# Performance work log

Hardware: AMD Instinct MI355X
Metric: run time of the kernel (lower is better)

Reference implementation:

```python
import jax, jax.numpy as jnp
import numpy as np

DIM = 768
NUM_HEADS = 12
HEAD_DIM = DIM // NUM_HEADS


def setup_inputs() -> dict:
    key = jax.random.key(0)
    k1, k2, k3 = jax.random.split(key, 3)
    B, N, C = 8, 4096, DIM
    x = jax.random.normal(k1, (B, N, C), dtype=jnp.float32)
    # torch nn.Linear weights are (out_features, in_features)
    W_qkv = jax.random.normal(k2, (3 * C, C), dtype=jnp.float32) * 0.02
    b_qkv = jnp.zeros((3 * C,), dtype=jnp.float32)
    W_proj = jax.random.normal(k3, (C, C), dtype=jnp.float32) * 0.02
    b_proj = jnp.zeros((C,), dtype=jnp.float32)
    return {"x": x, "W_qkv": W_qkv, "b_qkv": b_qkv, "W_proj": W_proj, "b_proj": b_proj}


def reference(x, W_qkv, b_qkv, W_proj, b_proj):
    B, N, C = x.shape
    H, D = NUM_HEADS, HEAD_DIM
    # qkv projection -> (3, B, H, N, D)
    qkv = (x @ W_qkv.T + b_qkv).reshape(B, N, 3, H, D).transpose(2, 0, 3, 1, 4)
    q, k, v = qkv[0], qkv[1], qkv[2]
    # feature map: elu(x) + 1 (positive kernel features)
    q = jax.nn.elu(q) + 1.0
    k = jax.nn.elu(k) + 1.0
    # kernelized linear attention: (K^T V) then Q (K^T V)
    kv = jnp.einsum('bhnd,bhnv->bhdv', k, v)          # (B,H,D,D)
    out = jnp.einsum('bhnd,bhdv->bhnv', q, kv)        # (B,H,N,D)
    k_sum = k.sum(axis=2)                             # (B,H,D)
    normalizer = jnp.einsum('bhnd,bhd->bhn', q, k_sum) + 1e-06
    out = out / normalizer[..., None]
    out = out.transpose(0, 2, 1, 3).reshape(B, N, C)
    out = out @ W_proj.T + b_proj
    return out
```

## Files before the change

### kernel.cpp

```cpp
#include <hip/hip_runtime.h>
#include <hip/hip_fp16.h>
#include <math.h>

#define NHEADS 12
#define SEQ 4096
#define BATCH 8

typedef _Float16 half8 __attribute__((ext_vector_type(8)));
typedef float floatx4 __attribute__((ext_vector_type(4)));

__global__ void zero_kernel(float* p, int n) {
  int i = blockIdx.x * 256 + threadIdx.x;
  if (i < n) p[i] = 0.f;
}

__global__ void cast_f2h(const float* __restrict__ in, __half* __restrict__ out, int n) {
  int i = (blockIdx.x * 256 + threadIdx.x) * 4;
  if (i < n) {
    float4 v = *(const float4*)&in[i];
    ushort4 o;
    o.x = __half_as_ushort(__float2half(v.x));
    o.y = __half_as_ushort(__float2half(v.y));
    o.z = __half_as_ushort(__float2half(v.z));
    o.w = __half_as_ushort(__float2half(v.w));
    *(ushort4*)&out[i] = o;
  }
}

__device__ __forceinline__ void stage_tile(const __half* __restrict__ gbase, int ldg,
                                           _Float16* lds, int t) {
#pragma unroll
  for (int it = 0; it < 2; ++it) {
    const int s  = it * 256 + t;
    const int mp = s >> 3, ps = s & 7;
    const int p  = ps ^ (mp & 7);
    const int r  = mp * 2 + (p >> 2);
    const int q  = p & 3;
    const __half* g = gbase + (size_t)r * ldg + q * 8;
    _Float16* dst = lds + (s >> 6) * 512;
    __builtin_amdgcn_global_load_lds((const __attribute__((address_space(1))) void*)g,
                                     (__attribute__((address_space(3))) void*)dst, 16, 0, 0);
  }
}
__device__ __forceinline__ void stage_blk(const __half* __restrict__ gbase, int ldg,
                                          _Float16* lds, int t) {
  const int mp = t >> 3, ps = t & 7;
  const int p  = ps ^ (mp & 7);
  const int r  = mp * 2 + (p >> 2);
  const int q  = p & 3;
  const __half* g = gbase + (size_t)r * ldg + q * 8;
  _Float16* dst = lds + (t >> 6) * 512;
  __builtin_amdgcn_global_load_lds((const __attribute__((address_space(1))) void*)g,
                                   (__attribute__((address_space(3))) void*)dst, 16, 0, 0);
}
__device__ __forceinline__ half8 read_frag(const _Float16* lds, int row, int quad) {
  const int mp = row >> 1;
  const int p  = ((row & 1) << 2) | quad;
  const int ps = p ^ (mp & 7);
  return *(const half8*)(lds + (mp * 8 + ps) * 8);
}

__device__ __forceinline__ void write_l64(_Float16* lds, int row, int col, float v) {
  lds[row * 64 + ((((col >> 3) ^ (row & 7))) << 3) + (col & 7)] = (_Float16)v;
}
__device__ __forceinline__ half8 read_l64c(const _Float16* lds, int row, int c) {
  return *(const half8*)(lds + row * 64 + ((c ^ (row & 7)) << 3));
}

__device__ __forceinline__ void barrier_raw() {
  asm volatile("s_barrier" ::: "memory");
}

template<int MODE>
__global__ __launch_bounds__(512, 2) void hgemm256_kernel(
    const __half* __restrict__ A, const __half* __restrict__ W,
    const float* __restrict__ bias,
    __half* __restrict__ outK, __half* __restrict__ outV,
    float* __restrict__ outF, int colBase)
{
  const int K = 768;
  const int NT = 24;
  extern __shared__ __align__(16) _Float16 sh[];
  const int t    = threadIdx.x;
  const int w    = t >> 6;
  const int l    = t & 63;
  const int quad = l >> 4;
  const int mrow = l & 15;
  const int wm   = w >> 2;
  const int wn   = w & 3;

  constexpr int JB = (MODE == 1) ? 6 : 3;
  const int bid  = blockIdx.x;
  const int xcd  = bid & 7;
  const int ii   = bid >> 3;
  const int mg   = ii / JB;
  const int jj   = ii - mg * JB;
  const int m0   = (xcd * 16 + mg) * 256;
  const int j0   = jj * 256;

  floatx4 acc[8][4];
#pragma unroll
  for (int i = 0; i < 8; ++i)
#pragma unroll
    for (int j = 0; j < 4; ++j) acc[i][j] = (floatx4){0.f, 0.f, 0.f, 0.f};

#pragma unroll
  for (int kt = 0; kt < 3; ++kt) {
    _Float16* db = sh + kt * 16384;
    const int kg = kt * 32;
    stage_blk(A + (size_t)m0 * K + kg, K, db, t);
    stage_blk(A + (size_t)(m0 + 128) * K + kg, K, db + 4096, t);
    stage_blk(W + (size_t)(colBase + j0) * K + kg, K, db + 8192, t);
    stage_blk(W + (size_t)(colBase + j0 + 128) * K + kg, K, db + 12288, t);
  }
  asm volatile("s_waitcnt vmcnt(8)" ::: "memory");
  barrier_raw();

#pragma unroll 4
  for (int kt = 0; kt < NT; ++kt) {
    const _Float16* bb = sh + (kt & 3) * 16384;
    const bool st = (kt + 3 < NT);
    _Float16* db = sh + ((kt + 3) & 3) * 16384;
    const int kg = (kt + 3) * 32;
    half8 af[4], bf[4];

#pragma unroll
    for (int j = 0; j < 4; ++j) {
      const int C = wn * 64 + j * 16 + mrow;
      bf[j] = read_frag(bb + 8192 + (C >> 7) * 4096, C & 127, quad);
    }
#pragma unroll
    for (int i = 0; i < 4; ++i)
      af[i] = read_frag(bb + wm * 4096, i * 16 + mrow, quad);
    if (st) {
      stage_blk(A + (size_t)m0 * K + kg, K, db, t);
      stage_blk(A + (size_t)(m0 + 128) * K + kg, K, db + 4096, t);
    }
#pragma unroll
    for (int i = 0; i < 4; ++i)
#pragma unroll
      for (int j = 0; j < 4; ++j)
        acc[i][j] = __builtin_amdgcn_mfma_f32_16x16x32_f16(af[i], bf[j], acc[i][j], 0, 0, 0);

#pragma unroll
    for (int i = 0; i < 4; ++i)
      af[i] = read_frag(bb + wm * 4096, (i + 4) * 16 + mrow, quad);
    if (st) {
      stage_blk(W + (size_t)(colBase + j0) * K + kg, K, db + 8192, t);
      stage_blk(W + (size_t)(colBase + j0 + 128) * K + kg, K, db + 12288, t);
    }
#pragma unroll
    for (int i = 0; i < 4; ++i)
#pragma unroll
      for (int j = 0; j < 4; ++j)
        acc[i + 4][j] = __builtin_amdgcn_mfma_f32_16x16x32_f16(af[i], bf[j], acc[i + 4][j], 0, 0, 0);

    if (kt < NT - 3)       asm volatile("s_waitcnt vmcnt(8)" ::: "memory");
    else if (kt == NT - 3) asm volatile("s_waitcnt vmcnt(4)" ::: "memory");
    else if (kt == NT - 2) asm volatile("s_waitcnt vmcnt(0)" ::: "memory");
    barrier_raw();
  }

  if (MODE == 0) {
#pragma unroll
    for (int j = 0; j < 4; ++j) {
      const int col = j0 + wn * 64 + j * 16 + mrow;
      const float bsv = bias[col];
#pragma unroll
      for (int i = 0; i < 8; ++i)
#pragma unroll
        for (int r = 0; r < 4; ++r) {
          const int m = m0 + wm * 128 + i * 16 + quad * 4 + r;
          outF[(size_t)m * 768 + col] = acc[i][j][r] + bsv;
        }
    }
    return;
  }

  const int col0 = colBase + j0 + wn * 64;
  const int t3   = col0 / 768;
  const int h    = (col0 - t3 * 768) >> 6;
  __half* dst    = (t3 == 1) ? outK : outV;
  const int m0w  = m0 + wm * 128;
  const int b_   = m0w >> 12;
  const int n0w  = m0w & 4095;
  _Float16* scr  = sh + w * 4096;

#pragma unroll
  for (int hf = 0; hf < 2; ++hf) {
#pragma unroll
    for (int j = 0; j < 4; ++j) {
      const int col = j * 16 + mrow;
      const float bsv = bias[col0 + col];
#pragma unroll
      for (int ii2 = 0; ii2 < 4; ++ii2)
#pragma unroll
        for (int r = 0; r < 4; ++r) {
          const int row = ii2 * 16 + quad * 4 + r;
          float val = acc[hf * 4 + ii2][j][r] + bsv;
          if (t3 == 1) val = (val > 0.f) ? (val + 1.f) : expf(val);
          write_l64(scr, row, col, val);
        }
    }
    barrier_raw();
    const size_t gb = ((size_t)(b_ * NHEADS + h) * SEQ + n0w + hf * 64) * 64;
#pragma unroll
    for (int it = 0; it < 8; ++it) {
      const int row = it * 8 + (l >> 3);
      const int c   = l & 7;
      half8 vv = read_l64c(scr, row, c);
      *(half8*)((_Float16*)dst + gb + (size_t)row * 64 + c * 8) = vv;
    }
    barrier_raw();
  }
}

__global__ __launch_bounds__(256) void kv_kernel(
    const __half* __restrict__ k, const __half* __restrict__ v,
    float* __restrict__ kv, float* __restrict__ ksum)
{
  __shared__ float ks[32 * 64];
  __shared__ float vs[32 * 64];
  const int bh = blockIdx.x;
  const int s  = blockIdx.y;
  const int t  = threadIdx.x;
  const int w  = t >> 6;
  const int l  = t & 63;
  const size_t base = (size_t)bh * SEQ * 64 + (size_t)s * 512 * 64;

  float acc[16];
#pragma unroll
  for (int i = 0; i < 16; ++i) acc[i] = 0.f;
  float kspart = 0.f;

  const int nn0 = t >> 3;
  const int c8  = (t & 7) * 8;

  for (int chunk = 0; chunk < 512; chunk += 32) {
    __syncthreads();
    {
      half8 kk = *(const half8*)&k[base + (size_t)(chunk + nn0) * 64 + c8];
      half8 vv = *(const half8*)&v[base + (size_t)(chunk + nn0) * 64 + c8];
#pragma unroll
      for (int e = 0; e < 8; ++e) {
        ks[nn0 * 64 + c8 + e] = (float)kk[e];
        vs[nn0 * 64 + c8 + e] = (float)vv[e];
      }
    }
    __syncthreads();
#pragma unroll 4
    for (int nn = 0; nn < 32; ++nn) {
      const float ve = vs[nn * 64 + l];
      const float4* kr = (const float4*)&ks[nn * 64 + w * 16];
      float4 k0 = kr[0], k1 = kr[1], k2 = kr[2], k3 = kr[3];
      acc[0]  += k0.x * ve; acc[1]  += k0.y * ve; acc[2]  += k0.z * ve; acc[3]  += k0.w * ve;
      acc[4]  += k1.x * ve; acc[5]  += k1.y * ve; acc[6]  += k1.z * ve; acc[7]  += k1.w * ve;
      acc[8]  += k2.x * ve; acc[9]  += k2.y * ve; acc[10] += k2.z * ve; acc[11] += k2.w * ve;
      acc[12] += k3.x * ve; acc[13] += k3.y * ve; acc[14] += k3.z * ve; acc[15] += k3.w * ve;
      kspart += ks[nn * 64 + l];
    }
  }
#pragma unroll
  for (int i = 0; i < 16; ++i) {
    const int d = w * 16 + i;
    atomicAdd(&kv[((size_t)bh * 64 + d) * 64 + l], acc[i]);
  }
  if (t < 64) atomicAdd(&ksum[(size_t)bh * 64 + l], kspart);
}

__global__ __launch_bounds__(256) void qattn_kernel(
    const __half* __restrict__ A, const __half* __restrict__ W,
    const float* __restrict__ bias,
    const float* __restrict__ kvg, const float* __restrict__ ksumg,
    __half* __restrict__ att)
{
  const int K = 768;
  __shared__ __align__(16) _Float16 sh[24576];
  _Float16* As = sh;
  _Float16* Bs = sh + 4096;
  __shared__ float norms[256];
  __shared__ float ksums[128];
  const int t    = threadIdx.x;
  const int w    = t >> 6;
  const int l    = t & 63;
  const int quad = l >> 4;
  const int mrow = l & 15;
  const int m0   = blockIdx.x * 128;
  const int j0   = blockIdx.y * 128;
  const int wr   = (w >> 1) * 64;
  const int wc   = (w & 1) * 64;
  const int b_   = m0 >> 12;
  const int h0   = j0 >> 6;

  {
    _Float16* kvT0 = sh + 16384;
#pragma unroll
    for (int ii = 0; ii < 32; ++ii) {
      const int gidx = ii * 256 + t;
      const int head = gidx >> 12;
      const int r    = gidx & 4095;
      const float val = kvg[(size_t)(b_ * NHEADS + h0 + head) * 4096 + r];
      write_l64(kvT0 + head * 4096, r & 63, r >> 6, val);
    }
    if (t < 128) ksums[t] = ksumg[(size_t)(b_ * NHEADS + h0 + (t >> 6)) * 64 + (t & 63)];
  }

  floatx4 acc[4][4];
#pragma unroll
  for (int i = 0; i < 4; ++i)
#pragma unroll
    for (int j = 0; j < 4; ++j) acc[i][j] = (floatx4){0.f, 0.f, 0.f, 0.f};

  for (int k0 = 0; k0 < K; k0 += 32) {
    __syncthreads();
    stage_tile(A + (size_t)m0 * K + k0, K, As, t);
    stage_tile(W + (size_t)j0 * K + k0, K, Bs, t);
    __syncthreads();
    half8 af[4], bf[4];
#pragma unroll
    for (int i = 0; i < 4; ++i) af[i] = read_frag(As, wr + i * 16 + mrow, quad);
#pragma unroll
    for (int j = 0; j < 4; ++j) bf[j] = read_frag(Bs, wc + j * 16 + mrow, quad);
#pragma unroll
    for (int i = 0; i < 4; ++i)
#pragma unroll
      for (int j = 0; j < 4; ++j)
        acc[i][j] = __builtin_amdgcn_mfma_f32_16x16x32_f16(af[i], bf[j], acc[i][j], 0, 0, 0);
  }

  _Float16* qtile = sh + w * 4096;
  const _Float16* kvT = sh + 16384 + (w & 1) * 4096;
  const int hh = w & 1;

  __syncthreads();
#pragma unroll
  for (int j = 0; j < 4; ++j) {
    const int col = j * 16 + mrow;
    const float bsv = bias[j0 + wc + col];
#pragma unroll
    for (int i = 0; i < 4; ++i)
#pragma unroll
      for (int r = 0; r < 4; ++r) {
        const int row = i * 16 + quad * 4 + r;
        float val = acc[i][j][r] + bsv;
        val = (val > 0.f) ? (val + 1.f) : expf(val);
        write_l64(qtile, row, col, val);
      }
  }
  __syncthreads();

  {
    float nrm = 0.f;
#pragma unroll
    for (int c = 0; c < 8; ++c) {
      half8 qv = read_l64c(qtile, l, c);
#pragma unroll
      for (int e = 0; e < 8; ++e) nrm += (float)qv[e] * ksums[hh * 64 + c * 8 + e];
    }
    norms[w * 64 + l] = 1.f / (nrm + 1e-6f);
  }

  floatx4 oacc[4][4];
#pragma unroll
  for (int i = 0; i < 4; ++i)
#pragma unroll
    for (int j = 0; j < 4; ++j) oacc[i][j] = (floatx4){0.f, 0.f, 0.f, 0.f};
#pragma unroll
  for (int ks = 0; ks < 2; ++ks) {
    half8 af[4], bf[4];
#pragma unroll
    for (int i = 0; i < 4; ++i) af[i] = read_l64c(qtile, i * 16 + mrow, ks * 4 + quad);
#pragma unroll
    for (int j = 0; j < 4; ++j) bf[j] = read_l64c(kvT, j * 16 + mrow, ks * 4 + quad);
#pragma unroll
    for (int i = 0; i < 4; ++i)
#pragma unroll
      for (int j = 0; j < 4; ++j)
        oacc[i][j] = __builtin_amdgcn_mfma_f32_16x16x32_f16(af[i], bf[j], oacc[i][j], 0, 0, 0);
  }
  __syncthreads();

#pragma unroll
  for (int i = 0; i < 4; ++i)
#pragma unroll
    for (int r = 0; r < 4; ++r) {
      const int row = i * 16 + quad * 4 + r;
      const float rn = norms[w * 64 + row];
#pragma unroll
      for (int j = 0; j < 4; ++j)
        write_l64(qtile, row, j * 16 + mrow, oacc[i][j][r] * rn);
    }
  __syncthreads();
  const int n0w = (m0 & 4095) + wr;
  const size_t abase = (size_t)(b_ * SEQ + n0w) * 768 + (h0 + hh) * 64;
#pragma unroll
  for (int it = 0; it < 8; ++it) {
    const int row = it * 8 + (l >> 3);
    const int c   = l & 7;
    half8 vv = read_l64c(qtile, row, c);
    *(half8*)((_Float16*)att + abase + (size_t)row * 768 + c * 8) = vv;
  }
}

extern "C" void kernel_launch(void* const* d_in, const int* in_sizes, int n_in,
                              void* d_out, int out_size, void* d_ws, size_t ws_size,
                              hipStream_t stream)
{
  const float* x     = (const float*)d_in[0];
  const float* Wqkv  = (const float*)d_in[1];
  const float* bqkv  = (const float*)d_in[2];
  const float* Wproj = (const float*)d_in[3];
  const float* bproj = (const float*)d_in[4];
  float* out = (float*)d_out;

  const size_t SZ = (size_t)BATCH * NHEADS * SEQ * 64;
  __half* xh  = (__half*)d_ws;
  __half* Wqh = xh + SZ;
  __half* Wph = Wqh + (size_t)2304 * 768;
  __half* R3  = Wph + (size_t)768 * 768;
  __half* R4  = R3 + SZ;
  float*  kvb = (float*)(R4 + SZ);
  float*  ksum = kvb + 96 * 64 * 64;

  static bool attr_set = false;
  if (!attr_set) {
    hipFuncSetAttribute((const void*)hgemm256_kernel<1>,
                        hipFuncAttributeMaxDynamicSharedMemorySize, 131072);
    hipFuncSetAttribute((const void*)hgemm256_kernel<0>,
                        hipFuncAttributeMaxDynamicSharedMemorySize, 131072);
    attr_set = true;
  }

  zero_kernel<<<1560, 256, 0, stream>>>(kvb, 96 * 64 * 64 + 96 * 64);

  cast_f2h<<<(int)(SZ / 1024), 256, 0, stream>>>(x, xh, (int)SZ);
  cast_f2h<<<(2304 * 768) / 1024, 256, 0, stream>>>(Wqkv, Wqh, 2304 * 768);
  cast_f2h<<<(768 * 768) / 1024, 256, 0, stream>>>(Wproj, Wph, 768 * 768);

  hgemm256_kernel<1><<<768, 512, 131072, stream>>>(
      xh, Wqh, bqkv, R3, R4, nullptr, 768);

  kv_kernel<<<dim3(96, 8), 256, 0, stream>>>(R3, R4, kvb, ksum);

  qattn_kernel<<<dim3(256, 6), 256, 0, stream>>>(
      xh, Wqh, bqkv, kvb, ksum, R3);

  hgemm256_kernel<0><<<384, 512, 131072, stream>>>(
      R3, Wph, bproj, nullptr, nullptr, out, 0);
}
```

Measured before the change: 479.5 us.

## Store K/V transposed and compute K^T V with MFMA instructions

The QKV GEMM epilogue now writes K and V in a transposed (head-dim major, sequence minor) layout. A new kv kernel reads that layout directly into MFMA fp16 fragments and computes K^T V, plus the K row sums through an MFMA against a ones vector, replacing the scalar FP32 LDS-based outer-product loop. Per-wave partials are reduced in shared memory before the atomics. The transposed global stores may be less coalesced in the epilogue, and the new grid has fewer blocks.

```diff
diff --git a/kernel.cpp b/kernel.cpp
--- a/kernel.cpp
+++ b/kernel.cpp
@@ -185,6 +185,7 @@
   const int b_   = m0w >> 12;
   const int n0w  = m0w & 4095;
   _Float16* scr  = sh + w * 4096;
+  const size_t gbT = (size_t)(b_ * NHEADS + h) * 64 * 4096;
 
 #pragma unroll
   for (int hf = 0; hf < 2; ++hf) {
@@ -199,73 +200,98 @@
           const int row = ii2 * 16 + quad * 4 + r;
           float val = acc[hf * 4 + ii2][j][r] + bsv;
           if (t3 == 1) val = (val > 0.f) ? (val + 1.f) : expf(val);
-          write_l64(scr, row, col, val);
+          write_l64(scr, col, row, val);
         }
     }
     barrier_raw();
-    const size_t gb = ((size_t)(b_ * NHEADS + h) * SEQ + n0w + hf * 64) * 64;
 #pragma unroll
     for (int it = 0; it < 8; ++it) {
-      const int row = it * 8 + (l >> 3);
-      const int c   = l & 7;
-      half8 vv = read_l64c(scr, row, c);
-      *(half8*)((_Float16*)dst + gb + (size_t)row * 64 + c * 8) = vv;
+      const int dd = it * 8 + (l >> 3);
+      const int c  = l & 7;
+      half8 vv = read_l64c(scr, dd, c);
+      *(half8*)((_Float16*)dst + gbT + (size_t)dd * 4096 + n0w + hf * 64 + c * 8) = vv;
     }
     barrier_raw();
   }
 }
 
-__global__ __launch_bounds__(256) void kv_kernel(
-    const __half* __restrict__ k, const __half* __restrict__ v,
+__global__ __launch_bounds__(256) void kv_mfma_kernel(
+    const __half* __restrict__ kT, const __half* __restrict__ vT,
     float* __restrict__ kv, float* __restrict__ ksum)
 {
-  __shared__ float ks[32 * 64];
-  __shared__ float vs[32 * 64];
+  extern __shared__ float red[];
+  float* ksr = red + 4 * 4096;
   const int bh = blockIdx.x;
-  const int s  = blockIdx.y;
+  const int sp = blockIdx.y;
   const int t  = threadIdx.x;
   const int w  = t >> 6;
   const int l  = t & 63;
-  const size_t base = (size_t)bh * SEQ * 64 + (size_t)s * 512 * 64;
-
-  float acc[16];
-#pragma unroll
-  for (int i = 0; i < 16; ++i) acc[i] = 0.f;
-  float kspart = 0.f;
-
-  const int nn0 = t >> 3;
-  const int c8  = (t & 7) * 8;
-
-  for (int chunk = 0; chunk < 512; chunk += 32) {
-    __syncthreads();
-    {
-      half8 kk = *(const half8*)&k[base + (size_t)(chunk + nn0) * 64 + c8];
-      half8 vv = *(const half8*)&v[base + (size_t)(chunk + nn0) * 64 + c8];
-#pragma unroll
-      for (int e = 0; e < 8; ++e) {
-        ks[nn0 * 64 + c8 + e] = (float)kk[e];
-        vs[nn0 * 64 + c8 + e] = (float)vv[e];
-      }
-    }
-    __syncthreads();
-#pragma unroll 4
-    for (int nn = 0; nn < 32; ++nn) {
-      const float ve = vs[nn * 64 + l];
-      const float4* kr = (const float4*)&ks[nn * 64 + w * 16];
-      float4 k0 = kr[0], k1 = kr[1], k2 = kr[2], k3 = kr[3];
-      acc[0]  += k0.x * ve; acc[1]  += k0.y * ve; acc[2]  += k0.z * ve; acc[3]  += k0.w * ve;
-      acc[4]  += k1.x * ve; acc[5]  += k1.y * ve; acc[6]  += k1.z * ve; acc[7]  += k1.w * ve;
-      acc[8]  += k2.x * ve; acc[9]  += k2.y * ve; acc[10] += k2.z * ve; acc[11] += k2.w * ve;
-      acc[12] += k3.x * ve; acc[13] += k3.y * ve; acc[14] += k3.z * ve; acc[15] += k3.w * ve;
-      kspart += ks[nn * 64 + l];
-    }
-  }
-#pragma unroll
-  for (int i = 0; i < 16; ++i) {
-    const int d = w * 16 + i;
-    atomicAdd(&kv[((size_t)bh * 64 + d) * 64 + l], acc[i]);
-  }
-  if (t < 64) atomicAdd(&ksum[(size_t)bh * 64 + l], kspart);
+  const int quad = l >> 4;
+  const int mrow = l & 15;
+  const size_t base = (size_t)bh * 64 * 4096;
+  const int n0 = sp * 1024 + w * 256;
+
+  floatx4 acc[4][4];
+  floatx4 ks[4];
+#pragma unroll
+  for (int i = 0; i < 4; ++i) {
+    ks[i] = (floatx4){0.f, 0.f, 0.f, 0.f};
+#pragma unroll
+    for (int j = 0; j < 4; ++j) acc[i][j] = (floatx4){0.f, 0.f, 0.f, 0.f};
+  }
+  half8 ones;
+#pragma unroll
+  for (int e = 0; e < 8; ++e) ones[e] = (_Float16)1.0f;
+
+  const __half* pk[4];
+  const __half* pv[4];
+#pragma unroll
+  for (int i = 0; i < 4; ++i) {
+    pk[i] = kT + base + (size_t)(i * 16 + mrow) * 4096 + n0 + quad * 8;
+    pv[i] = vT + base + (size_t)(i * 16 + mrow) * 4096 + n0 + quad * 8;
+  }
+
+#pragma unroll
+  for (int nn = 0; nn < 256; nn += 32) {
+    half8 af[4], bf[4];
+#pragma unroll
+    for (int i = 0; i < 4; ++i) af[i] = *(const half8*)(pk[i] + nn);
+#pragma unroll
+    for (int j = 0; j < 4; ++j) bf[j] = *(const half8*)(pv[j] + nn);
+#pragma unroll
+    for (int i = 0; i < 4; ++i)
+#pragma unroll
+      for (int j = 0; j < 4; ++j)
+        acc[i][j] = __builtin_amdgcn_mfma_f32_16x16x32_f16(af[i], bf[j], acc[i][j], 0, 0, 0);
+#pragma unroll
+    for (int i = 0; i < 4; ++i)
+      ks[i] = __builtin_amdgcn_mfma_f32_16x16x32_f16(af[i], ones, ks[i], 0, 0, 0);
+  }
+
+  float* rw = red + w * 4096;
+#pragma unroll
+  for (int i = 0; i < 4; ++i)
+#pragma unroll
+    for (int j = 0; j < 4; ++j)
+#pragma unroll
+      for (int r = 0; r < 4; ++r)
+        rw[(i * 16 + quad * 4 + r) * 64 + j * 16 + mrow] = acc[i][j][r];
+  if (mrow == 0) {
+#pragma unroll
+    for (int i = 0; i < 4; ++i)
+#pragma unroll
+      for (int r = 0; r < 4; ++r)
+        ksr[w * 64 + i * 16 + quad * 4 + r] = ks[i][r];
+  }
+  __syncthreads();
+#pragma unroll
+  for (int ii = 0; ii < 16; ++ii) {
+    const int idx = ii * 256 + t;
+    const float s = red[idx] + red[4096 + idx] + red[8192 + idx] + red[12288 + idx];
+    atomicAdd(&kv[(size_t)bh * 4096 + idx], s);
+  }
+  if (t < 64)
+    atomicAdd(&ksum[(size_t)bh * 64 + t], ksr[t] + ksr[64 + t] + ksr[128 + t] + ksr[192 + t]);
 }
 
 __global__ __launch_bounds__(256) void qattn_kernel(
@@ -428,6 +454,8 @@
                         hipFuncAttributeMaxDynamicSharedMemorySize, 131072);
     hipFuncSetAttribute((const void*)hgemm256_kernel<0>,
                         hipFuncAttributeMaxDynamicSharedMemorySize, 131072);
+    hipFuncSetAttribute((const void*)kv_mfma_kernel,
+                        hipFuncAttributeMaxDynamicSharedMemorySize, 66560);
     attr_set = true;
   }
 
@@ -440,7 +468,7 @@
   hgemm256_kernel<1><<<768, 512, 131072, stream>>>(
       xh, Wqh, bqkv, R3, R4, nullptr, 768);
 
-  kv_kernel<<<dim3(96, 8), 256, 0, stream>>>(R3, R4, kvb, ksum);
+  kv_mfma_kernel<<<dim3(96, 4), 256, 66560, stream>>>(R3, R4, kvb, ksum);
 
   qattn_kernel<<<dim3(256, 6), 256, 0, stream>>>(
       xh, Wqh, bqkv, kvb, ksum, R3);
```

Result: faster. 440.9 us (-8.1%).
